# Kernel tuning notes

Measured on AMD Instinct MI355X. Metric: run time of the kernel, lower is better.

The kernel has to match this reference:

```python
import jax, jax.numpy as jnp
import numpy as np

B, T, D, U = 2048, 200, 128, 128  # batch, history len, input dim, gru units


def setup_inputs() -> dict:
    key = jax.random.key(0)
    ks = jax.random.split(key, 5)
    s = 1.0 / np.sqrt(U + D)
    return {
        "history_state": jax.random.normal(ks[0], (B, T, D), jnp.float32),
        "attention_score": jax.random.uniform(ks[1], (B, T, 1), jnp.float32),
        "Wu": jax.random.normal(ks[2], (U + D, U), jnp.float32) * s,
        "bu": jnp.zeros((U,), jnp.float32),
        "Wr": jax.random.normal(ks[3], (U + D, U), jnp.float32) * s,
        "br": jnp.zeros((U,), jnp.float32),
        "Wh": jax.random.normal(ks[4], (D + U, U), jnp.float32) * s,
        "bh": jnp.zeros((U,), jnp.float32),
    }


def reference(history_state, attention_score, Wu, bu, Wr, br, Wh, bh):
    # time-major for scan: (T, B, ...)
    xs = jnp.swapaxes(history_state, 0, 1)       # (T, B, D)
    ats = jnp.swapaxes(attention_score, 0, 1)    # (T, B, 1)
    h0 = jnp.zeros((history_state.shape[0], Wu.shape[1]), history_state.dtype)

    def step(h, xa):
        x, a = xa
        hx = jnp.concatenate([h, x], axis=-1)                       # (B, U+D)
        u = jax.nn.sigmoid(hx @ Wu + bu)                            # update gate
        r = jax.nn.sigmoid(hx @ Wr + br)                            # reset gate
        hh = jnp.tanh(jnp.concatenate([x, r * h], axis=-1) @ Wh + bh)
        u = u * a                                                   # attention-modulated update
        h_new = u * hh + (1.0 - u) * h
        return h_new, None

    h_final, _ = jax.lax.scan(step, h0, (xs, ats))
    return h_final  # (B, U)
```

## Files before the change

### kernel.cpp

```cpp
#include <hip/hip_runtime.h>


#define T_LEN 200
#define D_DIM 128
#define U_DIM 128
#define BM    16
#define CH    12

typedef __attribute__((ext_vector_type(8))) short bf16x8;
typedef __attribute__((ext_vector_type(4))) float f32x4;

static __device__ __forceinline__ unsigned short f2bf(float f) {
    unsigned int u = __builtin_bit_cast(unsigned int, f);
    u += 0x7fffu + ((u >> 16) & 1u);
    return (unsigned short)(u >> 16);
}
static __device__ __forceinline__ bf16x8 pack8(float4 lo, float4 hi) {
    bf16x8 v;
    v[0] = (short)f2bf(lo.x); v[1] = (short)f2bf(lo.y);
    v[2] = (short)f2bf(lo.z); v[3] = (short)f2bf(lo.w);
    v[4] = (short)f2bf(hi.x); v[5] = (short)f2bf(hi.y);
    v[6] = (short)f2bf(hi.z); v[7] = (short)f2bf(hi.w);
    return v;
}
static __device__ __forceinline__ unsigned int pkbf2(float a, float b) {
    return (unsigned int)f2bf(a) | ((unsigned int)f2bf(b) << 16);
}
static __device__ __forceinline__ float fast_exp2(float x) {
#if __has_builtin(__builtin_amdgcn_exp2f)
    return __builtin_amdgcn_exp2f(x);
#else
    return exp2f(x);
#endif
}
static __device__ __forceinline__ float fast_rcp(float x) {
#if __has_builtin(__builtin_amdgcn_rcpf)
    return __builtin_amdgcn_rcpf(x);
#else
    return 1.0f / x;
#endif
}
static __device__ __forceinline__ int swz(int row, int c) {
    return row * 128 + ((c ^ (row & 7)) << 3);
}

__global__ __launch_bounds__(512, 2)
void gru_scan_kernel(const float* __restrict__ X,
                     const float* __restrict__ Att,
                     const float* __restrict__ Wu, const float* __restrict__ bu,
                     const float* __restrict__ Wr, const float* __restrict__ br,
                     const float* __restrict__ Wh, const float* __restrict__ bh,
                     float* __restrict__ out)
{
    __shared__ __align__(16) unsigned short x_sm[CH * BM * 128];
    __shared__ __align__(16) unsigned short h_bf[BM * 128];
    __shared__ __align__(16) unsigned short rh_bf[BM * 128];
    __shared__ float a_sm[CH * BM];

    const int tid  = threadIdx.x;
    const int wave = tid >> 6;
    const int lane = tid & 63;
    const int q    = lane >> 4;
    const int ln   = lane & 15;
    const int b0   = blockIdx.x * BM;

    const float INVLN2 = 1.4426950408889634f;

    bf16x8 wu[8], wr[8], wh[8];
    f32x4 nbu, nbr, bh2;
    {
        const int tb = 16 * wave;
        const int c  = tb + ln;
        const f32x4 bu4 = *(const f32x4*)&bu[tb + 4 * q];
        const f32x4 br4 = *(const f32x4*)&br[tb + 4 * q];
        const f32x4 bh4 = *(const f32x4*)&bh[tb + 4 * q];
        #pragma unroll
        for (int r = 0; r < 4; ++r) {
            nbu[r] = -bu4[r] * INVLN2;
            nbr[r] = -br4[r] * INVLN2;
            bh2[r] = 2.0f * bh4[r] * INVLN2;
        }
        #pragma unroll
        for (int kt = 0; kt < 8; ++kt) {
            const int k0 = 32 * kt + 8 * q;
            bf16x8 vu, vr, vh;
            #pragma unroll
            for (int j = 0; j < 8; ++j) {
                vu[j] = (short)f2bf(Wu[(k0 + j) * U_DIM + c] * -INVLN2);
                vr[j] = (short)f2bf(Wr[(k0 + j) * U_DIM + c] * -INVLN2);
                vh[j] = (short)f2bf(Wh[(k0 + j) * U_DIM + c] * (2.0f * INVLN2));
            }
            wu[kt] = vu; wr[kt] = vr; wh[kt] = vh;
        }
    }

    float hreg[4];
    #pragma unroll
    for (int r = 0; r < 4; ++r) hreg[r] = 0.0f;
    {
        unsigned int* hz = (unsigned int*)h_bf;
        if (tid < BM * 128 / 2 - 512) hz[tid + 512] = 0;
        hz[tid] = 0;
    }

    const int s2   = tid >> 8;
    const int srow = (tid >> 4) & 15;
    const int cs   = tid & 15;
    const float* xbase = X + (size_t)(b0 + srow) * T_LEN * D_DIM + cs * 8;

    int t0 = 0;
    for (int ch = 0; ch < (T_LEN + CH - 1) / CH; ++ch) {
        const int L = (t0 + CH <= T_LEN) ? CH : (T_LEN - t0);

        float4 px[12];
        #pragma unroll
        for (int w2 = 0; w2 < CH / 2; ++w2) {
            int t = t0 + 2 * w2 + s2;
            t = (t < T_LEN) ? t : (T_LEN - 1);
            const float* src = xbase + (size_t)t * D_DIM;
            px[2 * w2]     = *(const float4*)(src);
            px[2 * w2 + 1] = *(const float4*)(src + 4);
        }
        #pragma unroll
        for (int w2 = 0; w2 < CH / 2; ++w2) {
            const int s = 2 * w2 + s2;
            *(bf16x8*)&x_sm[swz(s * BM + srow, cs)] = pack8(px[2 * w2], px[2 * w2 + 1]);
        }
        if (tid < BM * CH) {
            int t = t0 + (tid >> 4);
            t = (t < T_LEN) ? t : (T_LEN - 1);
            a_sm[tid] = Att[(size_t)(b0 + (tid & 15)) * T_LEN + t];
        }
        __syncthreads();

        for (int s = 0; s < L; ++s) {
            bf16x8 hf[4], xf[4];
            #pragma unroll
            for (int kt = 0; kt < 4; ++kt) {
                hf[kt] = *(const bf16x8*)&h_bf[swz(ln, 4 * kt + q)];
                xf[kt] = *(const bf16x8*)&x_sm[swz(s * BM + ln, 4 * kt + q)];
            }
            const float a_att = a_sm[s * BM + ln];

            f32x4 accr1 = (f32x4)0.0f, accr2 = (f32x4)0.0f;
            f32x4 accu1 = (f32x4)0.0f, accu2 = (f32x4)0.0f;
            f32x4 acch  = (f32x4)0.0f;
            #pragma unroll
            for (int kt = 0; kt < 4; ++kt) {
                accr1 = __builtin_amdgcn_mfma_f32_16x16x32_bf16(wr[kt],     hf[kt], accr1, 0, 0, 0);
                accr2 = __builtin_amdgcn_mfma_f32_16x16x32_bf16(wr[kt + 4], xf[kt], accr2, 0, 0, 0);
            }
            #pragma unroll
            for (int kt = 0; kt < 4; ++kt) {
                acch  = __builtin_amdgcn_mfma_f32_16x16x32_bf16(wh[kt],     xf[kt], acch,  0, 0, 0);
                accu1 = __builtin_amdgcn_mfma_f32_16x16x32_bf16(wu[kt],     hf[kt], accu1, 0, 0, 0);
                accu2 = __builtin_amdgcn_mfma_f32_16x16x32_bf16(wu[kt + 4], xf[kt], accu2, 0, 0, 0);
            }

            {
                float rh[4];
                #pragma unroll
                for (int r = 0; r < 4; ++r) {
                    float zr = accr1[r] + accr2[r] + nbr[r];
                    float rv = fast_rcp(1.0f + fast_exp2(zr));
                    rh[r] = rv * hreg[r];
                }
                uint2 wv; wv.x = pkbf2(rh[0], rh[1]); wv.y = pkbf2(rh[2], rh[3]);
                const int c8 = 2 * wave + (q >> 1);
                *(uint2*)&rh_bf[ln * 128 + ((c8 ^ (ln & 7)) << 3) + (q & 1) * 4] = wv;
            }
            __syncthreads();

            bf16x8 rf[4];
            #pragma unroll
            for (int kt = 0; kt < 4; ++kt)
                rf[kt] = *(const bf16x8*)&rh_bf[swz(ln, 4 * kt + q)];

            float uq[4];
            #pragma unroll
            for (int r = 0; r < 4; ++r) {
                float zu = accu1[r] + accu2[r] + nbu[r];
                float u  = fast_rcp(1.0f + fast_exp2(zu));
                uq[r] = u * a_att;
            }
            #pragma unroll
            for (int kt = 0; kt < 4; ++kt)
                acch = __builtin_amdgcn_mfma_f32_16x16x32_bf16(wh[kt + 4], rf[kt], acch, 0, 0, 0);

            #pragma unroll
            for (int r = 0; r < 4; ++r) {
                float z  = acch[r] + bh2[r];
                float hh = 1.0f - 2.0f * fast_rcp(1.0f + fast_exp2(z));
                float ho = hreg[r];
                hreg[r] = ho + uq[r] * (hh - ho);
            }
            {
                uint2 wv; wv.x = pkbf2(hreg[0], hreg[1]); wv.y = pkbf2(hreg[2], hreg[3]);
                const int c8 = 2 * wave + (q >> 1);
                *(uint2*)&h_bf[ln * 128 + ((c8 ^ (ln & 7)) << 3) + (q & 1) * 4] = wv;
            }
            __syncthreads();
        }
        t0 += CH;
    }

    {
        f32x4 v;
        #pragma unroll
        for (int r = 0; r < 4; ++r) v[r] = hreg[r];
        *(f32x4*)&out[(size_t)(b0 + ln) * U_DIM + 16 * wave + 4 * q] = v;
    }
}

extern "C" void kernel_launch(void* const* d_in, const int* in_sizes, int n_in,
                              void* d_out, int out_size, void* d_ws, size_t ws_size,
                              hipStream_t stream) {
    const float* X   = (const float*)d_in[0];
    const float* Att = (const float*)d_in[1];
    const float* Wu  = (const float*)d_in[2];
    const float* bu  = (const float*)d_in[3];
    const float* Wr  = (const float*)d_in[4];
    const float* br  = (const float*)d_in[5];
    const float* Wh  = (const float*)d_in[6];
    const float* bh  = (const float*)d_in[7];
    float* out = (float*)d_out;

    gru_scan_kernel<<<dim3(2048 / BM), dim3(512), 0, stream>>>(
        X, Att, Wu, bu, Wr, br, Wh, bh, out);
}
```

Before: 489.4 us.

## Precompute next step's input projections before barrier and split MFMA chains

Moves the x-dependent MFMAs for step s+1 (reset, update and candidate gates) into the tail of step s, before the barrier, so the serial h-dependent path only carries the h and r*h products. Biases are folded into the accumulator initialisation. The r and candidate chains are split into two independent accumulators to shorten dependent MFMA latency. LDS changes from an XOR swizzle to a k-major padded layout (stride 136), and bf16 packing uses the hip_bf16 intrinsic. These additions raise register pressure and LDS footprint slightly.

```diff
diff --git a/kernel.cpp b/kernel.cpp
--- a/kernel.cpp
+++ b/kernel.cpp
@@ -1,4 +1,5 @@
 #include <hip/hip_runtime.h>
+#include <hip/hip_bf16.h>
 
 
 #define T_LEN 200
@@ -6,25 +7,29 @@
 #define U_DIM 128
 #define BM    16
 #define CH    12
+#define KCS   136
+#define XSTEP (16 * KCS)
 
 typedef __attribute__((ext_vector_type(8))) short bf16x8;
 typedef __attribute__((ext_vector_type(4))) float f32x4;
+typedef __attribute__((ext_vector_type(4))) unsigned int uint4v;
 
 static __device__ __forceinline__ unsigned short f2bf(float f) {
     unsigned int u = __builtin_bit_cast(unsigned int, f);
     u += 0x7fffu + ((u >> 16) & 1u);
     return (unsigned short)(u >> 16);
 }
-static __device__ __forceinline__ bf16x8 pack8(float4 lo, float4 hi) {
-    bf16x8 v;
-    v[0] = (short)f2bf(lo.x); v[1] = (short)f2bf(lo.y);
-    v[2] = (short)f2bf(lo.z); v[3] = (short)f2bf(lo.w);
-    v[4] = (short)f2bf(hi.x); v[5] = (short)f2bf(hi.y);
-    v[6] = (short)f2bf(hi.z); v[7] = (short)f2bf(hi.w);
+static __device__ __forceinline__ unsigned int pkbf2(float a, float b) {
+    float2 t; t.x = a; t.y = b;
+    __hip_bfloat162 v = __float22bfloat162_rn(t);
+    unsigned int u; __builtin_memcpy(&u, &v, 4);
+    return u;
+}
+static __device__ __forceinline__ uint4v pack8u(float4 lo, float4 hi) {
+    uint4v v;
+    v[0] = pkbf2(lo.x, lo.y); v[1] = pkbf2(lo.z, lo.w);
+    v[2] = pkbf2(hi.x, hi.y); v[3] = pkbf2(hi.z, hi.w);
     return v;
-}
-static __device__ __forceinline__ unsigned int pkbf2(float a, float b) {
-    return (unsigned int)f2bf(a) | ((unsigned int)f2bf(b) << 16);
 }
 static __device__ __forceinline__ float fast_exp2(float x) {
 #if __has_builtin(__builtin_amdgcn_exp2f)
@@ -39,9 +44,6 @@
 #else
     return 1.0f / x;
 #endif
-}
-static __device__ __forceinline__ int swz(int row, int c) {
-    return row * 128 + ((c ^ (row & 7)) << 3);
 }
 
 __global__ __launch_bounds__(512, 2)
@@ -52,9 +54,9 @@
                      const float* __restrict__ Wh, const float* __restrict__ bh,
                      float* __restrict__ out)
 {
-    __shared__ __align__(16) unsigned short x_sm[CH * BM * 128];
-    __shared__ __align__(16) unsigned short h_bf[BM * 128];
-    __shared__ __align__(16) unsigned short rh_bf[BM * 128];
+    __shared__ __align__(16) unsigned short x_sm[CH * XSTEP];
+    __shared__ __align__(16) unsigned short h_bf[XSTEP];
+    __shared__ __align__(16) unsigned short rh_bf[XSTEP];
     __shared__ float a_sm[CH * BM];
 
     const int tid  = threadIdx.x;
@@ -94,13 +96,12 @@
         }
     }
 
-    float hreg[4];
-    #pragma unroll
-    for (int r = 0; r < 4; ++r) hreg[r] = 0.0f;
+    float hreg[4] = {0.f, 0.f, 0.f, 0.f};
+
     {
         unsigned int* hz = (unsigned int*)h_bf;
-        if (tid < BM * 128 / 2 - 512) hz[tid + 512] = 0;
-        hz[tid] = 0;
+        unsigned int* rz = (unsigned int*)rh_bf;
+        for (int i = tid; i < XSTEP / 2; i += 512) { hz[i] = 0; rz[i] = 0; }
     }
 
     const int s2   = tid >> 8;
@@ -112,84 +113,98 @@
     for (int ch = 0; ch < (T_LEN + CH - 1) / CH; ++ch) {
         const int L = (t0 + CH <= T_LEN) ? CH : (T_LEN - t0);
 
-        float4 px[12];
-        #pragma unroll
-        for (int w2 = 0; w2 < CH / 2; ++w2) {
-            int t = t0 + 2 * w2 + s2;
-            t = (t < T_LEN) ? t : (T_LEN - 1);
-            const float* src = xbase + (size_t)t * D_DIM;
-            px[2 * w2]     = *(const float4*)(src);
-            px[2 * w2 + 1] = *(const float4*)(src + 4);
-        }
-        #pragma unroll
-        for (int w2 = 0; w2 < CH / 2; ++w2) {
-            const int s = 2 * w2 + s2;
-            *(bf16x8*)&x_sm[swz(s * BM + srow, cs)] = pack8(px[2 * w2], px[2 * w2 + 1]);
-        }
-        if (tid < BM * CH) {
-            int t = t0 + (tid >> 4);
-            t = (t < T_LEN) ? t : (T_LEN - 1);
-            a_sm[tid] = Att[(size_t)(b0 + (tid & 15)) * T_LEN + t];
+        {
+            float4 px[12];
+            #pragma unroll
+            for (int w2 = 0; w2 < CH / 2; ++w2) {
+                int t = t0 + 2 * w2 + s2;
+                t = (t < T_LEN) ? t : (T_LEN - 1);
+                const float* src = xbase + (size_t)t * D_DIM;
+                px[2 * w2]     = *(const float4*)(src);
+                px[2 * w2 + 1] = *(const float4*)(src + 4);
+            }
+            float a_px = 0.0f;
+            if (tid < BM * CH) {
+                int t = t0 + (tid >> 4);
+                t = (t < T_LEN) ? t : (T_LEN - 1);
+                a_px = Att[(size_t)(b0 + (tid & 15)) * T_LEN + t];
+            }
+            #pragma unroll
+            for (int w2 = 0; w2 < CH / 2; ++w2) {
+                const int s = 2 * w2 + s2;
+                *(uint4v*)&x_sm[s * XSTEP + cs * KCS + srow * 8] =
+                    pack8u(px[2 * w2], px[2 * w2 + 1]);
+            }
+            if (tid < BM * CH) a_sm[tid] = a_px;
         }
         __syncthreads();
 
+        f32x4 acc_r, acc_u, acc_h;
+        {
+            bf16x8 xf[4];
+            #pragma unroll
+            for (int kt = 0; kt < 4; ++kt)
+                xf[kt] = *(const bf16x8*)&x_sm[(4 * kt + q) * KCS + ln * 8];
+            acc_r = nbr; acc_u = nbu; acc_h = bh2;
+            #pragma unroll
+            for (int kt = 0; kt < 4; ++kt) {
+                acc_r = __builtin_amdgcn_mfma_f32_16x16x32_bf16(wr[kt + 4], xf[kt], acc_r, 0, 0, 0);
+                acc_u = __builtin_amdgcn_mfma_f32_16x16x32_bf16(wu[kt + 4], xf[kt], acc_u, 0, 0, 0);
+                acc_h = __builtin_amdgcn_mfma_f32_16x16x32_bf16(wh[kt],     xf[kt], acc_h, 0, 0, 0);
+            }
+        }
+
         for (int s = 0; s < L; ++s) {
-            bf16x8 hf[4], xf[4];
-            #pragma unroll
-            for (int kt = 0; kt < 4; ++kt) {
-                hf[kt] = *(const bf16x8*)&h_bf[swz(ln, 4 * kt + q)];
-                xf[kt] = *(const bf16x8*)&x_sm[swz(s * BM + ln, 4 * kt + q)];
-            }
+            bf16x8 hf[4];
+            #pragma unroll
+            for (int kt = 0; kt < 4; ++kt)
+                hf[kt] = *(const bf16x8*)&h_bf[(4 * kt + q) * KCS + ln * 8];
             const float a_att = a_sm[s * BM + ln];
 
-            f32x4 accr1 = (f32x4)0.0f, accr2 = (f32x4)0.0f;
-            f32x4 accu1 = (f32x4)0.0f, accu2 = (f32x4)0.0f;
-            f32x4 acch  = (f32x4)0.0f;
-            #pragma unroll
-            for (int kt = 0; kt < 4; ++kt) {
-                accr1 = __builtin_amdgcn_mfma_f32_16x16x32_bf16(wr[kt],     hf[kt], accr1, 0, 0, 0);
-                accr2 = __builtin_amdgcn_mfma_f32_16x16x32_bf16(wr[kt + 4], xf[kt], accr2, 0, 0, 0);
-            }
-            #pragma unroll
-            for (int kt = 0; kt < 4; ++kt) {
-                acch  = __builtin_amdgcn_mfma_f32_16x16x32_bf16(wh[kt],     xf[kt], acch,  0, 0, 0);
-                accu1 = __builtin_amdgcn_mfma_f32_16x16x32_bf16(wu[kt],     hf[kt], accu1, 0, 0, 0);
-                accu2 = __builtin_amdgcn_mfma_f32_16x16x32_bf16(wu[kt + 4], xf[kt], accu2, 0, 0, 0);
-            }
+            f32x4 ra = acc_r, rb = (f32x4)0.0f;
+            ra = __builtin_amdgcn_mfma_f32_16x16x32_bf16(wr[0], hf[0], ra, 0, 0, 0);
+            rb = __builtin_amdgcn_mfma_f32_16x16x32_bf16(wr[2], hf[2], rb, 0, 0, 0);
+            ra = __builtin_amdgcn_mfma_f32_16x16x32_bf16(wr[1], hf[1], ra, 0, 0, 0);
+            rb = __builtin_amdgcn_mfma_f32_16x16x32_bf16(wr[3], hf[3], rb, 0, 0, 0);
+            #pragma unroll
+            for (int kt = 0; kt < 4; ++kt)
+                acc_u = __builtin_amdgcn_mfma_f32_16x16x32_bf16(wu[kt], hf[kt], acc_u, 0, 0, 0);
 
             {
                 float rh[4];
                 #pragma unroll
                 for (int r = 0; r < 4; ++r) {
-                    float zr = accr1[r] + accr2[r] + nbr[r];
+                    float zr = ra[r] + rb[r];
                     float rv = fast_rcp(1.0f + fast_exp2(zr));
                     rh[r] = rv * hreg[r];
                 }
                 uint2 wv; wv.x = pkbf2(rh[0], rh[1]); wv.y = pkbf2(rh[2], rh[3]);
                 const int c8 = 2 * wave + (q >> 1);
-                *(uint2*)&rh_bf[ln * 128 + ((c8 ^ (ln & 7)) << 3) + (q & 1) * 4] = wv;
+                *(uint2*)&rh_bf[c8 * KCS + ln * 8 + (q & 1) * 4] = wv;
             }
             __syncthreads();
 
             bf16x8 rf[4];
             #pragma unroll
             for (int kt = 0; kt < 4; ++kt)
-                rf[kt] = *(const bf16x8*)&rh_bf[swz(ln, 4 * kt + q)];
+                rf[kt] = *(const bf16x8*)&rh_bf[(4 * kt + q) * KCS + ln * 8];
 
             float uq[4];
             #pragma unroll
             for (int r = 0; r < 4; ++r) {
-                float zu = accu1[r] + accu2[r] + nbu[r];
-                float u  = fast_rcp(1.0f + fast_exp2(zu));
+                float u = fast_rcp(1.0f + fast_exp2(acc_u[r]));
                 uq[r] = u * a_att;
             }
-            #pragma unroll
-            for (int kt = 0; kt < 4; ++kt)
-                acch = __builtin_amdgcn_mfma_f32_16x16x32_bf16(wh[kt + 4], rf[kt], acch, 0, 0, 0);
+
+            f32x4 ha = acc_h, hb = (f32x4)0.0f;
+            ha = __builtin_amdgcn_mfma_f32_16x16x32_bf16(wh[4], rf[0], ha, 0, 0, 0);
+            hb = __builtin_amdgcn_mfma_f32_16x16x32_bf16(wh[6], rf[2], hb, 0, 0, 0);
+            ha = __builtin_amdgcn_mfma_f32_16x16x32_bf16(wh[5], rf[1], ha, 0, 0, 0);
+            hb = __builtin_amdgcn_mfma_f32_16x16x32_bf16(wh[7], rf[3], hb, 0, 0, 0);
 
             #pragma unroll
             for (int r = 0; r < 4; ++r) {
-                float z  = acch[r] + bh2[r];
+                float z  = ha[r] + hb[r];
                 float hh = 1.0f - 2.0f * fast_rcp(1.0f + fast_exp2(z));
                 float ho = hreg[r];
                 hreg[r] = ho + uq[r] * (hh - ho);
@@ -197,7 +212,21 @@
             {
                 uint2 wv; wv.x = pkbf2(hreg[0], hreg[1]); wv.y = pkbf2(hreg[2], hreg[3]);
                 const int c8 = 2 * wave + (q >> 1);
-                *(uint2*)&h_bf[ln * 128 + ((c8 ^ (ln & 7)) << 3) + (q & 1) * 4] = wv;
+                *(uint2*)&h_bf[c8 * KCS + ln * 8 + (q & 1) * 4] = wv;
+            }
+
+            if (s + 1 < L) {
+                bf16x8 xf[4];
+                #pragma unroll
+                for (int kt = 0; kt < 4; ++kt)
+                    xf[kt] = *(const bf16x8*)&x_sm[(s + 1) * XSTEP + (4 * kt + q) * KCS + ln * 8];
+                acc_r = nbr; acc_u = nbu; acc_h = bh2;
+                #pragma unroll
+                for (int kt = 0; kt < 4; ++kt) {
+                    acc_r = __builtin_amdgcn_mfma_f32_16x16x32_bf16(wr[kt + 4], xf[kt], acc_r, 0, 0, 0);
+                    acc_u = __builtin_amdgcn_mfma_f32_16x16x32_bf16(wu[kt + 4], xf[kt], acc_u, 0, 0, 0);
+                    acc_h = __builtin_amdgcn_mfma_f32_16x16x32_bf16(wh[kt],     xf[kt], acc_h, 0, 0, 0);
+                }
             }
             __syncthreads();
         }
```

Measured after the change: 457.2 us. 6.6% less time.
